# Kernel optimization log

Measured on AMD Instinct MI355X. Metric: run time of the kernel, lower is better.

Reference implementation:

```python
import jax, jax.numpy as jnp
import numpy as np

D = 128   # edge_feature_size
E = 128   # number of edges in edge_feature_s_list
B = 4096  # true_batch_size


def setup_inputs() -> dict:
    key = jax.random.key(0)
    k1, k2, k3, k4 = jax.random.split(key, 4)
    temporal_edge_feature = jax.random.normal(k1, (B, D), dtype=jnp.float32)
    edge_feature_s = jax.random.normal(k2, (E, B, D), dtype=jnp.float32)
    W = jax.random.normal(k3, (D, D), dtype=jnp.float32) * (1.0 / np.sqrt(D))
    b = jax.random.normal(k4, (D,), dtype=jnp.float32) * 0.01
    return {
        "true_batch_size": B,
        "temporal_edge_feature": temporal_edge_feature,
        "edge_feature_s": edge_feature_s,
        "W": W,
        "b": b,
    }


def reference(true_batch_size, temporal_edge_feature, edge_feature_s, W, b):
    # Linear projection (same weights applied to source and each edge)
    m_i = temporal_edge_feature @ W.T + b            # [B, D]
    m_j = jnp.einsum('ebd,fd->ebf', edge_feature_s, W) + b  # [E, B, D]
    # Per-(edge, batch) dot-product score
    e_ij = jnp.einsum('bd,ebd->eb', m_i, m_j)        # [E, B]
    # Plain sum-normalization over edges (NOT softmax, faithful to source)
    e_j_sum = jnp.sum(e_ij, axis=0, keepdims=True)   # [1, B]
    weights = e_ij / e_j_sum                         # [E, B]
    # Weighted edge features
    out = weights[:, :, None] * edge_feature_s       # [E, B, D]
    return out
```

## Files before the change

kernel.cpp:

```cpp
#include <hip/hip_runtime.h>

constexpr int D    = 128;
constexpr int E    = 128;
constexpr int BB   = 4096;
constexpr int ROWS = 8;


__global__ __launch_bounds__(256) void prep_kernel(
    const float* __restrict__ T, const float* __restrict__ W,
    const float* __restrict__ bias, float* out)
{
    __shared__ float Wl[D][D + 1];
    __shared__ float Tl[ROWS][D];
    __shared__ float biasl[D];
    __shared__ float m[2][D];
    __shared__ float partial[4];

    const int t  = threadIdx.x;
    const int b0 = blockIdx.x * ROWS;

    for (int i = t; i < D * D; i += 256)
        Wl[i >> 7][i & 127] = W[i];
    for (int i = t; i < ROWS * D; i += 256)
        Tl[i >> 7][i & 127] = T[b0 * D + i];
    if (t < D) biasl[t] = bias[t];
    __syncthreads();

    const int half = t >> 7;
    const int lid  = t & 127;

    for (int pair = 0; pair < ROWS / 2; ++pair) {
        const int bl = pair * 2 + half;
        float acc = biasl[lid];
        for (int d = 0; d < D; ++d) acc += Tl[bl][d] * Wl[lid][d];
        m[half][lid] = acc;
        float pc = acc * biasl[lid];
        #pragma unroll
        for (int msk = 32; msk >= 1; msk >>= 1) pc += __shfl_xor(pc, msk);
        if ((t & 63) == 0) partial[t >> 6] = pc;
        __syncthreads();
        float vacc = 0.f;
        for (int f = 0; f < D; ++f) vacc += m[half][f] * Wl[f][lid];
        out[(size_t)(b0 + bl) * D + lid] = vacc;
        if (lid == 0)
            out[(size_t)(BB + b0 + bl) * D] =
                partial[2 * half] + partial[2 * half + 1];
        __syncthreads();
    }
}

__global__ __launch_bounds__(256) void att_main(
    const float* __restrict__ S, float* out)
{
    const int b  = blockIdx.x;
    const int t  = threadIdx.x;
    const int lc = t & 31;
    const int eb = t >> 5;

    __shared__ float sc[E];
    __shared__ float inv_s;

    const float4* Sp = (const float4*)S;
    const float4  v4 = ((const float4*)(out + (size_t)b * D))[lc];
    const float   c  = out[(size_t)(BB + b) * D];

    float4 s[16];
    #pragma unroll
    for (int i = 0; i < 16; ++i) {
        const int e = i * 8 + eb;
        s[i] = Sp[((size_t)e * BB + b) * 32 + lc];
    }

    #pragma unroll
    for (int i = 0; i < 16; ++i) {
        float p = s[i].x * v4.x + s[i].y * v4.y + s[i].z * v4.z + s[i].w * v4.w;
        #pragma unroll
        for (int msk = 16; msk >= 1; msk >>= 1) p += __shfl_xor(p, msk);
        if (lc == 0) sc[i * 8 + eb] = p + c;
    }
    __syncthreads();

    if (t < 64) {
        double d0 = (double)sc[t] + (double)sc[t + 64];
        #pragma unroll
        for (int msk = 32; msk >= 1; msk >>= 1) d0 += __shfl_xor(d0, msk);
        if (t == 0) inv_s = (float)(1.0 / d0);
    }
    __syncthreads();

    const float inv = inv_s;
    #pragma unroll
    for (int i = 0; i < 16; ++i) {
        const int e = i * 8 + eb;
        const float w = sc[e] * inv;
        float4 o;
        o.x = s[i].x * w; o.y = s[i].y * w;
        o.z = s[i].z * w; o.w = s[i].w * w;
        ((float4*)out)[((size_t)e * BB + b) * 32 + lc] = o;
    }
}

extern "C" void kernel_launch(void* const* d_in, const int* in_sizes, int n_in,
                              void* d_out, int out_size, void* d_ws, size_t ws_size,
                              hipStream_t stream) {
    const float* T    = (const float*)d_in[1];
    const float* S    = (const float*)d_in[2];
    const float* W    = (const float*)d_in[3];
    const float* bias = (const float*)d_in[4];
    float* out        = (float*)d_out;

    prep_kernel<<<BB / ROWS, 256, 0, stream>>>(T, W, bias, out);
    att_main<<<BB, 256, 0, stream>>>(S, out);
}
```

Before: 472.7 us.

## Precompute Gram matrix W^T W and use nontemporal loads/stores in main kernel

Replaces the per-row two-stage projection with a precomputed Gram matrix G = W^T W, bias-projected vector h and b·b. A new small kernel writes these into scratch space inside the output buffer, and the prep kernel then computes v = T·G + h with register tiling and c = T·h + b². The main attention kernel switches to nontemporal loads and stores for the streaming edge features. This adds a third kernel launch and changes the order of floating-point summation.

After: 467.3 us. Within noise of the previous version (-1.1%).

```diff
diff --git a/kernel.cpp b/kernel.cpp
--- a/kernel.cpp
+++ b/kernel.cpp
@@ -5,48 +5,89 @@
 constexpr int BB   = 4096;
 constexpr int ROWS = 8;
 
+typedef float f32x4 __attribute__((ext_vector_type(4)));
 
-__global__ __launch_bounds__(256) void prep_kernel(
-    const float* __restrict__ T, const float* __restrict__ W,
-    const float* __restrict__ bias, float* out)
+
+__global__ __launch_bounds__(128) void gwh_kernel(
+    const float* __restrict__ W, const float* __restrict__ bias, float* out)
 {
-    __shared__ float Wl[D][D + 1];
+    __shared__ float Wl[D][D];
+    __shared__ float bl[D];
+    const int t = threadIdx.x;
+    const int r = blockIdx.x;
+
+    const float4* W4 = (const float4*)W;
+    float4* Wl4 = (float4*)&Wl[0][0];
+    for (int i = t; i < D * D / 4; i += 128) Wl4[i] = W4[i];
+    bl[t] = bias[t];
+    __syncthreads();
+
+    float acc = 0.f;
+    for (int k = 0; k < D; ++k) acc += Wl[k][r] * Wl[k][t];
+    out[(size_t)2 * BB * D + r * D + t] = acc;
+
+    if (r == 0) {
+        float hh = 0.f;
+        for (int f = 0; f < D; ++f) hh += bl[f] * Wl[f][t];
+        out[(size_t)3 * BB * D + t] = hh;
+        if (t == 0) {
+            float b2 = 0.f;
+            for (int f = 0; f < D; ++f) b2 += bl[f] * bl[f];
+            out[(size_t)3 * BB * D + D] = b2;
+        }
+    }
+}
+
+__global__ __launch_bounds__(256) void prep2_kernel(
+    const float* __restrict__ T, float* out)
+{
+    __shared__ float Gl[D][D];
     __shared__ float Tl[ROWS][D];
-    __shared__ float biasl[D];
-    __shared__ float m[2][D];
-    __shared__ float partial[4];
+    __shared__ float hl[D];
+    __shared__ float beta_s;
 
     const int t  = threadIdx.x;
     const int b0 = blockIdx.x * ROWS;
 
-    for (int i = t; i < D * D; i += 256)
-        Wl[i >> 7][i & 127] = W[i];
-    for (int i = t; i < ROWS * D; i += 256)
-        Tl[i >> 7][i & 127] = T[b0 * D + i];
-    if (t < D) biasl[t] = bias[t];
+    {
+        const float4* Gs = (const float4*)(out + (size_t)2 * BB * D);
+        float4* Gd = (float4*)&Gl[0][0];
+        for (int i = t; i < D * D / 4; i += 256) Gd[i] = Gs[i];
+        const float4* Ts = (const float4*)(T + (size_t)b0 * D);
+        ((float4*)&Tl[0][0])[t] = Ts[t];
+        if (t < D) hl[t] = out[(size_t)3 * BB * D + t];
+        if (t == 0) beta_s = out[(size_t)3 * BB * D + D];
+    }
     __syncthreads();
 
-    const int half = t >> 7;
-    const int lid  = t & 127;
+    const int dc = t & 127;
+    const int r0 = (t >> 7) * 4;
+    float a0 = hl[dc], a1 = hl[dc], a2 = hl[dc], a3 = hl[dc];
+    #pragma unroll 4
+    for (int k = 0; k < D; k += 4) {
+        const float g0 = Gl[k + 0][dc], g1 = Gl[k + 1][dc],
+                    g2 = Gl[k + 2][dc], g3 = Gl[k + 3][dc];
+        const float4 t0 = *(const float4*)&Tl[r0 + 0][k];
+        const float4 t1 = *(const float4*)&Tl[r0 + 1][k];
+        const float4 t2 = *(const float4*)&Tl[r0 + 2][k];
+        const float4 t3 = *(const float4*)&Tl[r0 + 3][k];
+        a0 += t0.x * g0 + t0.y * g1 + t0.z * g2 + t0.w * g3;
+        a1 += t1.x * g0 + t1.y * g1 + t1.z * g2 + t1.w * g3;
+        a2 += t2.x * g0 + t2.y * g1 + t2.z * g2 + t2.w * g3;
+        a3 += t3.x * g0 + t3.y * g1 + t3.z * g2 + t3.w * g3;
+    }
+    out[(size_t)(b0 + r0 + 0) * D + dc] = a0;
+    out[(size_t)(b0 + r0 + 1) * D + dc] = a1;
+    out[(size_t)(b0 + r0 + 2) * D + dc] = a2;
+    out[(size_t)(b0 + r0 + 3) * D + dc] = a3;
 
-    for (int pair = 0; pair < ROWS / 2; ++pair) {
-        const int bl = pair * 2 + half;
-        float acc = biasl[lid];
-        for (int d = 0; d < D; ++d) acc += Tl[bl][d] * Wl[lid][d];
-        m[half][lid] = acc;
-        float pc = acc * biasl[lid];
-        #pragma unroll
-        for (int msk = 32; msk >= 1; msk >>= 1) pc += __shfl_xor(pc, msk);
-        if ((t & 63) == 0) partial[t >> 6] = pc;
-        __syncthreads();
-        float vacc = 0.f;
-        for (int f = 0; f < D; ++f) vacc += m[half][f] * Wl[f][lid];
-        out[(size_t)(b0 + bl) * D + lid] = vacc;
-        if (lid == 0)
-            out[(size_t)(BB + b0 + bl) * D] =
-                partial[2 * half] + partial[2 * half + 1];
-        __syncthreads();
-    }
+    const int cr = t >> 5, cl = t & 31;
+    const float4 tc = *(const float4*)&Tl[cr][cl * 4];
+    const float4 hc = *(const float4*)&hl[cl * 4];
+    float p = tc.x * hc.x + tc.y * hc.y + tc.z * hc.z + tc.w * hc.w;
+    #pragma unroll
+    for (int msk = 16; msk >= 1; msk >>= 1) p += __shfl_xor(p, msk);
+    if (cl == 0) out[(size_t)(BB + b0 + cr) * D] = p + beta_s;
 }
 
 __global__ __launch_bounds__(256) void att_main(
@@ -60,15 +101,15 @@
     __shared__ float sc[E];
     __shared__ float inv_s;
 
-    const float4* Sp = (const float4*)S;
-    const float4  v4 = ((const float4*)(out + (size_t)b * D))[lc];
-    const float   c  = out[(size_t)(BB + b) * D];
+    const f32x4* Sp = (const f32x4*)S;
+    const f32x4  v4 = ((const f32x4*)(out + (size_t)b * D))[lc];
+    const float  c  = out[(size_t)(BB + b) * D];
 
-    float4 s[16];
+    f32x4 s[16];
     #pragma unroll
     for (int i = 0; i < 16; ++i) {
         const int e = i * 8 + eb;
-        s[i] = Sp[((size_t)e * BB + b) * 32 + lc];
+        s[i] = __builtin_nontemporal_load(Sp + ((size_t)e * BB + b) * 32 + lc);
     }
 
     #pragma unroll
@@ -89,14 +130,13 @@
     __syncthreads();
 
     const float inv = inv_s;
+    f32x4* Op = (f32x4*)out;
     #pragma unroll
     for (int i = 0; i < 16; ++i) {
         const int e = i * 8 + eb;
         const float w = sc[e] * inv;
-        float4 o;
-        o.x = s[i].x * w; o.y = s[i].y * w;
-        o.z = s[i].z * w; o.w = s[i].w * w;
-        ((float4*)out)[((size_t)e * BB + b) * 32 + lc] = o;
+        f32x4 o = s[i] * w;
+        __builtin_nontemporal_store(o, Op + ((size_t)e * BB + b) * 32 + lc);
     }
 }
 
@@ -109,6 +149,7 @@
     const float* bias = (const float*)d_in[4];
     float* out        = (float*)d_out;
 
-    prep_kernel<<<BB / ROWS, 256, 0, stream>>>(T, W, bias, out);
+    gwh_kernel<<<D, D, 0, stream>>>(W, bias, out);
+    prep2_kernel<<<BB / ROWS, 256, 0, stream>>>(T, out);
     att_main<<<BB, 256, 0, stream>>>(S, out);
 }
```
